# Kernel optimization log

Measured on AMD Instinct MI355X. Metric: run time of the kernel, lower is better.

The kernel has to match this reference:

```python
import jax, jax.numpy as jnp
import numpy as np

N_NODES = 10000
N_EDGES = 160000
N_FEAT = 512
HEADS = 8
HID = 128
OUT = 16


def setup_inputs() -> dict:
    key = jax.random.key(0)
    ks = jax.random.split(key, 16)
    inp = {
        'node_features': jax.random.normal(ks[0], (N_NODES, N_FEAT), jnp.float32),
        'edge_src': jax.random.randint(ks[1], (N_EDGES,), 0, N_NODES, jnp.int32),
        'edge_dst': jax.random.randint(ks[2], (N_EDGES,), 0, N_NODES, jnp.int32),
        # GAT layer params (scaled randn for numerical sanity)
        'W1': jax.random.normal(ks[3], (HEADS, HID, N_FEAT), jnp.float32) * 0.05,
        'a1': jax.random.normal(ks[4], (HEADS, 2 * HID), jnp.float32) * 0.05,
        'W2': jax.random.normal(ks[5], (HEADS, HID, HID), jnp.float32) * 0.05,
        'a2': jax.random.normal(ks[6], (HEADS, 2 * HID), jnp.float32) * 0.05,
        # MLP: LayerNorm(128) -> Linear(128,64) -> LeakyReLU -> Linear(64,16) -> LeakyReLU -> Linear(16,OUT) -> ReLU
        'ln_g': jnp.ones((HID,), jnp.float32),
        'ln_b': jnp.zeros((HID,), jnp.float32),
        'Wl1': jax.random.normal(ks[7], (64, HID), jnp.float32) * 0.05,
        'bl1': jnp.zeros((64,), jnp.float32),
        'Wl2': jax.random.normal(ks[8], (16, 64), jnp.float32) * 0.05,
        'bl2': jnp.zeros((16,), jnp.float32),
        'Wl3': jax.random.normal(ks[9], (OUT, 16), jnp.float32) * 0.05,
        'bl3': jnp.zeros((OUT,), jnp.float32),
    }
    return inp


def gat_layer(x, src, dst, W, a, n_nodes):
    # per-node, per-head projection: h[n,h,d]
    h = jnp.einsum('hdf,nf->nhd', W, x)
    # split attention vector: e_ij = a[:HID].h_i + a[HID:].h_j
    s_i = jnp.einsum('nhd,hd->nh', h, a[:, :HID])  # score contribution of target i
    s_j = jnp.einsum('nhd,hd->nh', h, a[:, HID:])  # score contribution of neighbor j
    e = jax.nn.leaky_relu(s_i[dst] + s_j[src])     # [E,H], negative_slope=0.01 (torch default)
    # segment softmax over edges grouped by dst
    m = jax.ops.segment_max(e, dst, num_segments=n_nodes)           # [N,H]
    m = jnp.where(jnp.isfinite(m), m, 0.0)
    ex = jnp.exp(e - m[dst])                                        # [E,H]
    denom = jax.ops.segment_sum(ex, dst, num_segments=n_nodes)      # [N,H]
    alpha = ex / jnp.where(denom > 0, denom, 1.0)[dst]              # [E,H]
    # scatter-accumulate weighted neighbor embeddings
    agg = jax.ops.segment_sum(alpha[:, :, None] * h[src], dst, num_segments=n_nodes)  # [N,H,HID]
    # average over heads, ELU (matches 1/attn_heads * attn_sum -> ELU)
    return jax.nn.elu(agg.mean(axis=1))  # [N,HID]


def reference(node_features, edge_src, edge_dst, W1, a1, W2, a2,
              ln_g, ln_b, Wl1, bl1, Wl2, bl2, Wl3, bl3):
    n = node_features.shape[0]
    emb1 = gat_layer(node_features, edge_src, edge_dst, W1, a1, n)
    emb2 = gat_layer(emb1, edge_src, edge_dst, W2, a2, n)
    g = emb2.mean(axis=0)  # [HID] graph embedding
    # MLP head (dropout = identity at inference)
    mu = g.mean()
    var = ((g - mu) ** 2).mean()
    gn = (g - mu) / jnp.sqrt(var + 1e-5) * ln_g + ln_b
    x = jax.nn.leaky_relu(Wl1 @ gn + bl1)
    x = jax.nn.leaky_relu(Wl2 @ x + bl2)
    return jax.nn.relu(Wl3 @ x + bl3)
```

## Files before the change

### kernel.cpp

```cpp
#include <hip/hip_runtime.h>
#include <math.h>

#define N_NODES 10000
#define N_EDGES 160000
#define N_FEAT  512
#define HEADS   8
#define HID     128

typedef __attribute__((ext_vector_type(8))) short bf16x8;
typedef __attribute__((ext_vector_type(4))) float f32x4;
typedef __attribute__((ext_vector_type(2))) float v2f;

__device__ inline unsigned short f2bf_rne(float f) {
  unsigned int u = __float_as_uint(f);
  unsigned int r = u + 0x7fffu + ((u >> 16) & 1u);
  return (unsigned short)(r >> 16);
}
__device__ inline float bf2f(unsigned int b) {
  return __uint_as_float(b << 16);
}

__device__ inline void split_body(const float* __restrict__ in,
                                  unsigned short* __restrict__ hi,
                                  int R, int K8, int idx) {
  int r = idx & 15;
  int t = idx >> 4;
  int kq = t % K8;
  int rb = t / K8;
  int row = rb * 16 + r;
  float v[8] = {0.f, 0.f, 0.f, 0.f, 0.f, 0.f, 0.f, 0.f};
  if (row < R) {
    const float* p = in + (size_t)row * (K8 * 8) + kq * 8;
    float4 a = *(const float4*)p;
    float4 b = *(const float4*)(p + 4);
    v[0] = a.x; v[1] = a.y; v[2] = a.z; v[3] = a.w;
    v[4] = b.x; v[5] = b.y; v[6] = b.z; v[7] = b.w;
  }
  union { unsigned short u[8]; int4 v4; } H;
  #pragma unroll
  for (int e = 0; e < 8; ++e) H.u[e] = f2bf_rne(v[e]);
  *(int4*)&hi[(size_t)idx * 8] = H.v4;
}

__global__ __launch_bounds__(256)
void split_frag2(const float* __restrict__ in1, unsigned short* __restrict__ hi1,
                 int R1, int K81, int total1, int nb1,
                 const float* __restrict__ in2, unsigned short* __restrict__ hi2,
                 int R2, int K82, int total2, int nb2,
                 const float* __restrict__ W2p, unsigned short* __restrict__ hi3,
                 int total3, int nb3,
                 const int* __restrict__ esrc, const int* __restrict__ edst,
                 int* __restrict__ deg, int* __restrict__ slots,
                 int2* __restrict__ ovf, int* __restrict__ cnt, int E,
                 const float* __restrict__ av1, const float* __restrict__ av2,
                 float* __restrict__ wt1, float* __restrict__ wt2) {
  int b = (int)blockIdx.x;
  int tid = threadIdx.x;
  if (b < nb1) {
    int idx = b * 256 + tid;
    if (idx < total1) split_body(in1, hi1, R1, K81, idx);
  } else if (b < nb1 + nb2) {
    int idx = (b - nb1) * 256 + tid;
    if (idx < total2) split_body(in2, hi2, R2, K82, idx);
  } else if (b < nb1 + nb2 + nb3) {
    int idx = (b - nb1 - nb2) * 256 + tid;
    if (idx < total3) split_body(W2p, hi3, HEADS * HID, 16, idx);
  } else {
    int nbE = (E + 255) / 256;
    int eb = b - nb1 - nb2 - nb3;
    if (eb < nbE) {
      int e = eb * 256 + tid;
      if (e < E) {
        int d = edst[e], s = esrc[e];
        int p = atomicAdd(&deg[d], 1);
        if (p < 32) {
          slots[d * 32 + p] = s;
        } else {
          int q = atomicAdd(&cnt[1], 1);
          if (q < E) ovf[q] = make_int2(d, s);
        }
      }
    } else {
      int wb = eb - nbE;
      if (wb < 32) {
        int o = wb * 256 + tid;
        int f = o & 511, ii = (o >> 9) & 1, h = o >> 10;
        const float* Wp = in2 + (size_t)h * HID * N_FEAT + f;
        const float* ap = av1 + h * 2 * HID + ii * HID;
        float c0 = 0.f, c1 = 0.f;
        for (int d = 0; d < HID; d += 2) {
          c0 = fmaf(Wp[(size_t)d * N_FEAT], ap[d], c0);
          c1 = fmaf(Wp[(size_t)(d + 1) * N_FEAT], ap[d + 1], c1);
        }
        wt1[o] = c0 + c1;
      } else {
        int o = (wb - 32) * 256 + tid;
        int f = o & 127, ii = (o >> 7) & 1, h = o >> 8;
        const float* Wp = W2p + (size_t)h * HID * HID + f;
        const float* ap = av2 + h * 2 * HID + ii * HID;
        float c0 = 0.f, c1 = 0.f;
        for (int d = 0; d < HID; d += 2) {
          c0 = fmaf(Wp[(size_t)d * HID], ap[d], c0);
          c1 = fmaf(Wp[(size_t)(d + 1) * HID], ap[d + 1], c1);
        }
        wt2[o] = c0 + c1;
      }
    }
  }
}

__global__ __launch_bounds__(256, 3)
void gemm_score(const unsigned short* __restrict__ Afh,
                const unsigned short* __restrict__ Bfh,
                unsigned short* __restrict__ hb,
                int M, int K, int nbGemm,
                const float* __restrict__ x, const float* __restrict__ wt1,
                float* __restrict__ si, float* __restrict__ sj, int N) {
  int tid = threadIdx.x;
  if ((int)blockIdx.x >= nbGemm) {
    __shared__ float wl[8192];
    #pragma unroll
    for (int k = 0; k < 32; ++k) wl[tid + k * 256] = wt1[tid + k * 256];
    __syncthreads();
    int wv = tid >> 6, lane = tid & 63;
    int rr = lane >> 4, sl = lane & 15;
    int n = ((int)blockIdx.x - nbGemm) * 16 + wv * 4 + rr;
    if (n >= N) return;
    const float* xp = x + (size_t)n * N_FEAT + sl * 4;
    float acc[16];
    #pragma unroll
    for (int t = 0; t < 16; ++t) acc[t] = 0.f;
    #pragma unroll
    for (int k = 0; k < 8; ++k) {
      float4 xv = *(const float4*)(xp + k * 64);
      #pragma unroll
      for (int t = 0; t < 16; ++t) {
        float4 w4 = *(const float4*)&wl[t * 512 + k * 64 + sl * 4];
        acc[t] = fmaf(xv.x, w4.x, fmaf(xv.y, w4.y, fmaf(xv.z, w4.z, fmaf(xv.w, w4.w, acc[t]))));
      }
    }
    #pragma unroll
    for (int o = 1; o <= 8; o <<= 1)
      #pragma unroll
      for (int t = 0; t < 16; ++t) acc[t] += __shfl_xor(acc[t], o);
    float outv = acc[0];
    #pragma unroll
    for (int t = 1; t < 16; ++t) outv = (sl == t) ? acc[t] : outv;
    int h = sl >> 1;
    if (sl & 1) sj[(size_t)h * N + n] = outv;
    else        si[(size_t)h * N + n] = outv;
    return;
  }

  int wave = tid >> 6, lane = tid & 63;
  int r = lane & 15, q = lane >> 4;
  int wr = wave >> 1, wc = wave & 1;

  int blk = blockIdx.x;
  int mtile = blk % 80;
  int head = blk / 80;
  int m0 = mtile * 128;
  int K8 = K >> 3;

  const bf16x8* pA = (const bf16x8*)Afh;
  const bf16x8* pB = (const bf16x8*)Bfh;
  size_t rstep = (size_t)K8 * 16;
  size_t aidx = (size_t)((m0 >> 4) + wr * 4) * rstep + (size_t)q * 16 + r;
  size_t bidx = (size_t)(head * 8 + wc * 4) * rstep + (size_t)q * 16 + r;

  f32x4 acc[4][4] = {};

  for (int k0 = 0; k0 < K; k0 += 64, aidx += 128, bidx += 128) {
    bf16x8 a[8], b[8];
    #pragma unroll
    for (int i = 0; i < 4; ++i) {
      a[i]     = pA[aidx + i * rstep];
      b[i]     = pB[bidx + i * rstep];
      a[i + 4] = pA[aidx + i * rstep + 64];
      b[i + 4] = pB[bidx + i * rstep + 64];
    }
    #pragma unroll
    for (int i = 0; i < 4; ++i)
      #pragma unroll
      for (int j = 0; j < 4; ++j)
        acc[i][j] = __builtin_amdgcn_mfma_f32_16x16x32_bf16(a[i], b[j], acc[i][j], 0, 0, 0);
    #pragma unroll
    for (int i = 0; i < 4; ++i)
      #pragma unroll
      for (int j = 0; j < 4; ++j)
        acc[i][j] = __builtin_amdgcn_mfma_f32_16x16x32_bf16(a[i + 4], b[j + 4], acc[i][j], 0, 0, 0);
  }

  #pragma unroll
  for (int i = 0; i < 4; ++i)
    #pragma unroll
    for (int reg = 0; reg < 4; ++reg) {
      int row = m0 + wr * 64 + i * 16 + q * 4 + reg;
      if (row < M) {
        #pragma unroll
        for (int j = 0; j < 4; ++j)
          hb[((size_t)head * M + row) * HID + wc * 64 + j * 16 + r] =
              f2bf_rne(acc[i][j][reg]);
      }
    }
}

__global__ __launch_bounds__(512)
void gat_aggregate9(const unsigned short* __restrict__ hb,
                    const float* __restrict__ si, const float* __restrict__ sj,
                    const int* __restrict__ deg, const int* __restrict__ slots,
                    const int2* __restrict__ ovf, const int* __restrict__ cnt,
                    unsigned short* __restrict__ aggb, int N) {
  __shared__ int2 prs[8][4][32];
  int head = blockIdx.x & 7;
  int wv = threadIdx.x >> 6;
  int lane = threadIdx.x & 63;
  int grp = lane >> 4;
  int sl = lane & 15;
  int n = (blockIdx.x >> 3) * 32 + wv * 4 + grp;
  const unsigned short* hbase = hb + (size_t)head * N * HID;
  const float* sjh = sj + (size_t)head * N;
  bool nv = n < N;
  int dg = 0;
  float s_i = 0.f;
  if (nv) {
    dg = deg[n];
    s_i = si[(size_t)head * N + n];
  }
  int sbase = n * 32;

  int src0 = 0, src1 = 0;
  float sc0 = -INFINITY, sc1 = -INFINITY;
  if (sl < dg) {
    src0 = slots[sbase + sl];
    float t = s_i + sjh[src0];
    sc0 = t > 0.f ? t : 0.01f * t;
  }
  if (16 + sl < dg) {
    src1 = slots[sbase + 16 + sl];
    float t = s_i + sjh[src1];
    sc1 = t > 0.f ? t : 0.01f * t;
  }
  float m = fmaxf(sc0, sc1);
  int oc = 0;
  if (dg > 32) {
    oc = cnt[1];
    if (oc > N_EDGES) oc = N_EDGES;
    for (int e2 = sl; e2 < oc; e2 += 16) {
      int2 pe = ovf[e2];
      if (pe.x == n) {
        float t = s_i + sjh[pe.y];
        t = t > 0.f ? t : 0.01f * t;
        m = fmaxf(m, t);
      }
    }
  }
  #pragma unroll
  for (int o = 1; o <= 8; o <<= 1) m = fmaxf(m, __shfl_xor(m, o));

  float w0 = (sl < dg) ? __expf(sc0 - m) : 0.f;
  float w1 = (16 + sl < dg) ? __expf(sc1 - m) : 0.f;
  float den = w0 + w1;
  if (dg > 32) {
    for (int e2 = sl; e2 < oc; e2 += 16) {
      int2 pe = ovf[e2];
      if (pe.x == n) {
        float t = s_i + sjh[pe.y];
        t = t > 0.f ? t : 0.01f * t;
        den += __expf(t - m);
      }
    }
  }
  #pragma unroll
  for (int o = 1; o <= 8; o <<= 1) den += __shfl_xor(den, o);

  prs[wv][grp][sl] = make_int2(src0, __float_as_int(w0));
  prs[wv][grp][16 + sl] = make_int2(src1, __float_as_int(w1));
  __asm__ volatile("s_waitcnt lgkmcnt(0)" ::: "memory");

  v2f a01 = {0.f, 0.f}, a23 = {0.f, 0.f}, a45 = {0.f, 0.f}, a67 = {0.f, 0.f};
  int dmin = dg < 32 ? dg : 32;
  for (int e0 = 0; e0 < dmin; e0 += 8) {
    int2 p[8];
    #pragma unroll
    for (int u = 0; u < 8; ++u) p[u] = prs[wv][grp][e0 + u];
    int4 pv[8];
    #pragma unroll
    for (int u = 0; u < 8; ++u)
      pv[u] = *(const int4*)&hbase[(size_t)p[u].x * HID + sl * 8];
    #pragma unroll
    for (int u = 0; u < 8; ++u) {
      float w = __int_as_float(p[u].y);
      v2f w2 = {w, w};
      int4 q = pv[u];
      v2f t0 = {bf2f((unsigned)q.x & 0xffffu), __uint_as_float((unsigned)q.x & 0xffff0000u)};
      v2f t1 = {bf2f((unsigned)q.y & 0xffffu), __uint_as_float((unsigned)q.y & 0xffff0000u)};
      v2f t2 = {bf2f((unsigned)q.z & 0xffffu), __uint_as_float((unsigned)q.z & 0xffff0000u)};
      v2f t3 = {bf2f((unsigned)q.w & 0xffffu), __uint_as_float((unsigned)q.w & 0xffff0000u)};
      a01 += w2 * t0;
      a23 += w2 * t1;
      a45 += w2 * t2;
      a67 += w2 * t3;
    }
  }
  if (dg > 32) {
    for (int e2 = 0; e2 < oc; ++e2) {
      int2 pe = ovf[e2];
      if (pe.x != n) continue;
      float t = s_i + sjh[pe.y];
      t = t > 0.f ? t : 0.01f * t;
      float w = __expf(t - m);
      v2f w2 = {w, w};
      int4 q = *(const int4*)&hbase[(size_t)pe.y * HID + sl * 8];
      v2f t0 = {bf2f((unsigned)q.x & 0xffffu), __uint_as_float((unsigned)q.x & 0xffff0000u)};
      v2f t1 = {bf2f((unsigned)q.y & 0xffffu), __uint_as_float((unsigned)q.y & 0xffff0000u)};
      v2f t2 = {bf2f((unsigned)q.z & 0xffffu), __uint_as_float((unsigned)q.z & 0xffff0000u)};
      v2f t3 = {bf2f((unsigned)q.w & 0xffffu), __uint_as_float((unsigned)q.w & 0xffff0000u)};
      a01 += w2 * t0; a23 += w2 * t1; a45 += w2 * t2; a67 += w2 * t3;
    }
  }

  if (nv) {
    float inv = den > 0.f ? 1.0f / den : 0.f;
    union { unsigned short u[8]; int4 v4; } P;
    P.u[0] = f2bf_rne(a01.x * inv); P.u[1] = f2bf_rne(a01.y * inv);
    P.u[2] = f2bf_rne(a23.x * inv); P.u[3] = f2bf_rne(a23.y * inv);
    P.u[4] = f2bf_rne(a45.x * inv); P.u[5] = f2bf_rne(a45.y * inv);
    P.u[6] = f2bf_rne(a67.x * inv); P.u[7] = f2bf_rne(a67.y * inv);
    *(int4*)&aggb[((size_t)head * N + n) * HID + sl * 8] = P.v4;
  }
}

__global__ __launch_bounds__(256)
void headmean_frag2(const unsigned short* __restrict__ aggb,
                    unsigned short* __restrict__ hiA, int N,
                    const float* __restrict__ wt2,
                    float* __restrict__ si, float* __restrict__ sj) {
  __shared__ float wl[2048];
  __shared__ float sred[16][16][17];
  int tid = threadIdx.x;
  #pragma unroll
  for (int k = 0; k < 8; ++k) wl[tid + k * 256] = wt2[tid + k * 256];
  __syncthreads();
  int idx = blockIdx.x * 256 + tid;
  int r = idx & 15;
  int kq = (idx >> 4) & 15;
  int rb = idx >> 8;
  int n = rb * 16 + r;
  float s[8] = {0.f, 0.f, 0.f, 0.f, 0.f, 0.f, 0.f, 0.f};
  if (n < N) {
    #pragma unroll
    for (int hh = 0; hh < HEADS; ++hh) {
      int4 pv = *(const int4*)&aggb[((size_t)hh * N + n) * HID + kq * 8];
      s[0] += bf2f((unsigned)pv.x & 0xffffu);
      s[1] += __uint_as_float((unsigned)pv.x & 0xffff0000u);
      s[2] += bf2f((unsigned)pv.y & 0xffffu);
      s[3] += __uint_as_float((unsigned)pv.y & 0xffff0000u);
      s[4] += bf2f((unsigned)pv.z & 0xffffu);
      s[5] += __uint_as_float((unsigned)pv.z & 0xffff0000u);
      s[6] += bf2f((unsigned)pv.w & 0xffffu);
      s[7] += __uint_as_float((unsigned)pv.w & 0xffff0000u);
    }
  }
  float p[16];
  #pragma unroll
  for (int t = 0; t < 16; ++t) p[t] = 0.f;
  union { unsigned short u[8]; int4 v4; } H;
  #pragma unroll
  for (int e = 0; e < 8; ++e) {
    float v = s[e] * (1.0f / HEADS);
    v = v > 0.f ? v : (__expf(v) - 1.0f);
    #pragma unroll
    for (int t = 0; t < 16; ++t) p[t] = fmaf(v, wl[t * 128 + kq * 8 + e], p[t]);
    H.u[e] = f2bf_rne(v);
  }
  *(int4*)&hiA[(size_t)idx * 8] = H.v4;
  #pragma unroll
  for (int t = 0; t < 16; ++t) sred[kq][r][t] = p[t];
  __syncthreads();
  {
    int rr = tid >> 4, t = tid & 15;
    float sum = 0.f;
    #pragma unroll
    for (int k = 0; k < 16; ++k) sum += sred[k][rr][t];
    int nn = rb * 16 + rr;
    if (nn < N) {
      int h = t >> 1;
      if (t & 1) sj[(size_t)h * N + nn] = sum;
      else       si[(size_t)h * N + nn] = sum;
    }
  }
}

__global__ __launch_bounds__(256)
void headmean_pool(const unsigned short* __restrict__ aggb, float* __restrict__ g,
                   int N) {
  __shared__ float sm[16][128];
  int t = threadIdx.x;
  int nl = t >> 4, dg = t & 15;
  int n = blockIdx.x * 16 + nl;
  float v[8] = {0.f, 0.f, 0.f, 0.f, 0.f, 0.f, 0.f, 0.f};
  if (n < N) {
    #pragma unroll
    for (int hh = 0; hh < HEADS; ++hh) {
      int4 pv = *(const int4*)&aggb[((size_t)hh * N + n) * HID + dg * 8];
      v[0] += bf2f((unsigned)pv.x & 0xffffu);
      v[1] += __uint_as_float((unsigned)pv.x & 0xffff0000u);
      v[2] += bf2f((unsigned)pv.y & 0xffffu);
      v[3] += __uint_as_float((unsigned)pv.y & 0xffff0000u);
      v[4] += bf2f((unsigned)pv.z & 0xffffu);
      v[5] += __uint_as_float((unsigned)pv.z & 0xffff0000u);
      v[6] += bf2f((unsigned)pv.w & 0xffffu);
      v[7] += __uint_as_float((unsigned)pv.w & 0xffff0000u);
    }
    #pragma unroll
    for (int e = 0; e < 8; ++e) {
      float x = v[e] * (1.0f / HEADS);
      v[e] = x > 0.f ? x : (__expf(x) - 1.0f);
    }
  }
  #pragma unroll
  for (int e = 0; e < 8; ++e) sm[nl][dg * 8 + e] = v[e];
  __syncthreads();
  if (t < 128) {
    float s = 0.f;
    #pragma unroll
    for (int nn = 0; nn < 16; ++nn) s += sm[nn][t];
    atomicAdd(&g[t], s);
  }
}

__global__ __launch_bounds__(128)
void mlp_kernel(const float* __restrict__ g, const float* __restrict__ ln_g,
                const float* __restrict__ ln_b, const float* __restrict__ Wl1,
                const float* __restrict__ bl1, const float* __restrict__ Wl2,
                const float* __restrict__ bl2, const float* __restrict__ Wl3,
                const float* __restrict__ bl3, float* __restrict__ out, float invN) {
  __shared__ float red[128];
  __shared__ float gn[128];
  __shared__ float x1[64];
  __shared__ float x2[16];
  int t = threadIdx.x;
  float gg = g[t] * invN;
  red[t] = gg;
  __syncthreads();
  for (int o = 64; o > 0; o >>= 1) {
    if (t < o) red[t] += red[t + o];
    __syncthreads();
  }
  float mu = red[0] * (1.0f / HID);
  __syncthreads();
  float dv = gg - mu;
  red[t] = dv * dv;
  __syncthreads();
  for (int o = 64; o > 0; o >>= 1) {
    if (t < o) red[t] += red[t + o];
    __syncthreads();
  }
  float var = red[0] * (1.0f / HID);
  gn[t] = dv / sqrtf(var + 1e-5f) * ln_g[t] + ln_b[t];
  __syncthreads();
  if (t < 64) {
    float s = bl1[t];
    for (int k = 0; k < 128; ++k) s += Wl1[t * 128 + k] * gn[k];
    x1[t] = s > 0.f ? s : 0.01f * s;
  }
  __syncthreads();
  if (t < 16) {
    float s = bl2[t];
    for (int k = 0; k < 64; ++k) s += Wl2[t * 64 + k] * x1[k];
    x2[t] = s > 0.f ? s : 0.01f * s;
  }
  __syncthreads();
  if (t < 16) {
    float s = bl3[t];
    for (int k = 0; k < 16; ++k) s += Wl3[t * 16 + k] * x2[k];
    out[t] = s > 0.f ? s : 0.f;
  }
}

extern "C" void kernel_launch(void* const* d_in, const int* in_sizes, int n_in,
                              void* d_out, int out_size, void* d_ws, size_t ws_size,
                              hipStream_t stream) {
  const float* x    = (const float*)d_in[0];
  const int*   esrc = (const int*)d_in[1];
  const int*   edst = (const int*)d_in[2];
  const float* W1   = (const float*)d_in[3];
  const float* a1   = (const float*)d_in[4];
  const float* W2   = (const float*)d_in[5];
  const float* a2   = (const float*)d_in[6];
  const float* ln_g = (const float*)d_in[7];
  const float* ln_b = (const float*)d_in[8];
  const float* Wl1  = (const float*)d_in[9];
  const float* bl1  = (const float*)d_in[10];
  const float* Wl2  = (const float*)d_in[11];
  const float* bl2  = (const float*)d_in[12];
  const float* Wl3  = (const float*)d_in[13];
  const float* bl3  = (const float*)d_in[14];
  float* out = (float*)d_out;

  const int RBPAD = 640;

  unsigned short* aggb = (unsigned short*)d_ws;
  float* si   = (float*)(aggb + (size_t)N_NODES * HEADS * HID);
  float* sj   = si + N_NODES * HEADS;
  float* g    = sj + N_NODES * HEADS;
  int*   deg  = (int*)(g + 128);
  int*   cnt  = deg + N_NODES;
  int*   slots= cnt + 4;
  int2*  ovf  = (int2*)(slots + (size_t)N_NODES * 32);
  float* wt1  = (float*)(ovf + N_EDGES);
  float* wt2  = wt1 + 8192;
  unsigned short* Afh  = (unsigned short*)(wt2 + 2048);
  unsigned short* Bfh  = Afh + (size_t)RBPAD * 64 * 128;
  unsigned short* Bfh2 = Bfh + (size_t)1024 * 512;
  unsigned short* hb   = Bfh2 + (size_t)1024 * 128;

  hipMemsetAsync(g, 0, 128 * sizeof(float) + (N_NODES + 4) * sizeof(int), stream);

  int gemmGrid = 80 * HEADS;
  int scoreGrid = (N_NODES + 15) / 16;
  int aggGrid = ((N_NODES + 31) / 32) * 8;

  {
    int totalA = RBPAD * 64 * 16;
    int nbA = (totalA + 255) / 256;
    int totalB = 64 * 64 * 16;
    int nbB = (totalB + 255) / 256;
    int totalB2 = 64 * 16 * 16;
    int nbB2 = (totalB2 + 255) / 256;
    int nbE = (N_EDGES + 255) / 256;
    int nbW = 40;
    split_frag2<<<nbA + nbB + nbB2 + nbE + nbW, 256, 0, stream>>>(
        x, Afh, N_NODES, 64, totalA, nbA,
        W1, Bfh, HEADS * HID, 64, totalB, nbB,
        W2, Bfh2, totalB2, nbB2,
        esrc, edst, deg, slots, ovf, cnt, N_EDGES,
        a1, a2, wt1, wt2);
  }

  gemm_score<<<gemmGrid + scoreGrid, 256, 0, stream>>>(
      Afh, Bfh, hb, N_NODES, N_FEAT, gemmGrid, x, wt1, si, sj, N_NODES);
  gat_aggregate9<<<aggGrid, 512, 0, stream>>>(hb, si, sj, deg, slots, ovf, cnt,
                                              aggb, N_NODES);
  headmean_frag2<<<(N_NODES + 15) / 16, 256, 0, stream>>>(aggb, Afh, N_NODES,
                                                          wt2, si, sj);

  gemm_score<<<gemmGrid, 256, 0, stream>>>(
      Afh, Bfh2, hb, N_NODES, HID, gemmGrid, nullptr, nullptr, nullptr, nullptr, 0);
  gat_aggregate9<<<aggGrid, 512, 0, stream>>>(hb, si, sj, deg, slots, ovf, cnt,
                                              aggb, N_NODES);

  headmean_pool<<<(N_NODES + 15) / 16, 256, 0, stream>>>(aggb, g, N_NODES);
  mlp_kernel<<<1, 128, 0, stream>>>(g, ln_g, ln_b, Wl1, bl1, Wl2, bl2, Wl3, bl3,
                                    out, 1.0f / N_NODES);
}
```

Baseline: 242.1 us.

## Fuse whole GAT pipeline into one persistent cooperative kernel with grid syncs

Replaces the seven separate kernel launches (prep/split, GEMM+score, aggregate, headmean, second GEMM, aggregate, pool, MLP) with a single cooperative persistent kernel of 256 or 512 blocks of 512 threads that loops over work items and separates phases with grid.sync(). The GEMM tile is reshaped for 8 waves per block (each wave now computes 32 rows instead of 64). The aim is to remove launch gaps and inter-kernel idle time. In exchange, the fixed grid may reduce parallelism in some phases, grid-wide barriers add cost, and the occupancy-dependent grid size carries risk.

```diff
diff --git a/kernel.cpp b/kernel.cpp
--- a/kernel.cpp
+++ b/kernel.cpp
@@ -1,5 +1,8 @@
 #include <hip/hip_runtime.h>
+#include <hip/hip_cooperative_groups.h>
 #include <math.h>
+
+namespace cg = cooperative_groups;
 
 #define N_NODES 10000
 #define N_EDGES 160000
@@ -42,160 +45,52 @@
   *(int4*)&hi[(size_t)idx * 8] = H.v4;
 }
 
-__global__ __launch_bounds__(256)
-void split_frag2(const float* __restrict__ in1, unsigned short* __restrict__ hi1,
-                 int R1, int K81, int total1, int nb1,
-                 const float* __restrict__ in2, unsigned short* __restrict__ hi2,
-                 int R2, int K82, int total2, int nb2,
-                 const float* __restrict__ W2p, unsigned short* __restrict__ hi3,
-                 int total3, int nb3,
-                 const int* __restrict__ esrc, const int* __restrict__ edst,
-                 int* __restrict__ deg, int* __restrict__ slots,
-                 int2* __restrict__ ovf, int* __restrict__ cnt, int E,
-                 const float* __restrict__ av1, const float* __restrict__ av2,
-                 float* __restrict__ wt1, float* __restrict__ wt2) {
-  int b = (int)blockIdx.x;
-  int tid = threadIdx.x;
-  if (b < nb1) {
-    int idx = b * 256 + tid;
-    if (idx < total1) split_body(in1, hi1, R1, K81, idx);
-  } else if (b < nb1 + nb2) {
-    int idx = (b - nb1) * 256 + tid;
-    if (idx < total2) split_body(in2, hi2, R2, K82, idx);
-  } else if (b < nb1 + nb2 + nb3) {
-    int idx = (b - nb1 - nb2) * 256 + tid;
-    if (idx < total3) split_body(W2p, hi3, HEADS * HID, 16, idx);
-  } else {
-    int nbE = (E + 255) / 256;
-    int eb = b - nb1 - nb2 - nb3;
-    if (eb < nbE) {
-      int e = eb * 256 + tid;
-      if (e < E) {
-        int d = edst[e], s = esrc[e];
-        int p = atomicAdd(&deg[d], 1);
-        if (p < 32) {
-          slots[d * 32 + p] = s;
-        } else {
-          int q = atomicAdd(&cnt[1], 1);
-          if (q < E) ovf[q] = make_int2(d, s);
-        }
-      }
-    } else {
-      int wb = eb - nbE;
-      if (wb < 32) {
-        int o = wb * 256 + tid;
-        int f = o & 511, ii = (o >> 9) & 1, h = o >> 10;
-        const float* Wp = in2 + (size_t)h * HID * N_FEAT + f;
-        const float* ap = av1 + h * 2 * HID + ii * HID;
-        float c0 = 0.f, c1 = 0.f;
-        for (int d = 0; d < HID; d += 2) {
-          c0 = fmaf(Wp[(size_t)d * N_FEAT], ap[d], c0);
-          c1 = fmaf(Wp[(size_t)(d + 1) * N_FEAT], ap[d + 1], c1);
-        }
-        wt1[o] = c0 + c1;
-      } else {
-        int o = (wb - 32) * 256 + tid;
-        int f = o & 127, ii = (o >> 7) & 1, h = o >> 8;
-        const float* Wp = W2p + (size_t)h * HID * HID + f;
-        const float* ap = av2 + h * 2 * HID + ii * HID;
-        float c0 = 0.f, c1 = 0.f;
-        for (int d = 0; d < HID; d += 2) {
-          c0 = fmaf(Wp[(size_t)d * HID], ap[d], c0);
-          c1 = fmaf(Wp[(size_t)(d + 1) * HID], ap[d + 1], c1);
-        }
-        wt2[o] = c0 + c1;
-      }
-    }
-  }
-}
-
-__global__ __launch_bounds__(256, 3)
-void gemm_score(const unsigned short* __restrict__ Afh,
-                const unsigned short* __restrict__ Bfh,
-                unsigned short* __restrict__ hb,
-                int M, int K, int nbGemm,
-                const float* __restrict__ x, const float* __restrict__ wt1,
-                float* __restrict__ si, float* __restrict__ sj, int N) {
-  int tid = threadIdx.x;
-  if ((int)blockIdx.x >= nbGemm) {
-    __shared__ float wl[8192];
-    #pragma unroll
-    for (int k = 0; k < 32; ++k) wl[tid + k * 256] = wt1[tid + k * 256];
-    __syncthreads();
-    int wv = tid >> 6, lane = tid & 63;
-    int rr = lane >> 4, sl = lane & 15;
-    int n = ((int)blockIdx.x - nbGemm) * 16 + wv * 4 + rr;
-    if (n >= N) return;
-    const float* xp = x + (size_t)n * N_FEAT + sl * 4;
-    float acc[16];
-    #pragma unroll
-    for (int t = 0; t < 16; ++t) acc[t] = 0.f;
-    #pragma unroll
-    for (int k = 0; k < 8; ++k) {
-      float4 xv = *(const float4*)(xp + k * 64);
-      #pragma unroll
-      for (int t = 0; t < 16; ++t) {
-        float4 w4 = *(const float4*)&wl[t * 512 + k * 64 + sl * 4];
-        acc[t] = fmaf(xv.x, w4.x, fmaf(xv.y, w4.y, fmaf(xv.z, w4.z, fmaf(xv.w, w4.w, acc[t]))));
-      }
-    }
-    #pragma unroll
-    for (int o = 1; o <= 8; o <<= 1)
-      #pragma unroll
-      for (int t = 0; t < 16; ++t) acc[t] += __shfl_xor(acc[t], o);
-    float outv = acc[0];
-    #pragma unroll
-    for (int t = 1; t < 16; ++t) outv = (sl == t) ? acc[t] : outv;
-    int h = sl >> 1;
-    if (sl & 1) sj[(size_t)h * N + n] = outv;
-    else        si[(size_t)h * N + n] = outv;
-    return;
-  }
-
+__device__ inline void gemm_tile_8w(const bf16x8* __restrict__ pA,
+                                    const bf16x8* __restrict__ pB,
+                                    unsigned short* __restrict__ hb,
+                                    int M, int K, int tile, int tid) {
   int wave = tid >> 6, lane = tid & 63;
   int r = lane & 15, q = lane >> 4;
   int wr = wave >> 1, wc = wave & 1;
-
-  int blk = blockIdx.x;
-  int mtile = blk % 80;
-  int head = blk / 80;
+  int mtile = tile % 80;
+  int head = tile / 80;
   int m0 = mtile * 128;
   int K8 = K >> 3;
-
-  const bf16x8* pA = (const bf16x8*)Afh;
-  const bf16x8* pB = (const bf16x8*)Bfh;
   size_t rstep = (size_t)K8 * 16;
-  size_t aidx = (size_t)((m0 >> 4) + wr * 4) * rstep + (size_t)q * 16 + r;
+  size_t aidx = (size_t)((m0 >> 4) + wr * 2) * rstep + (size_t)q * 16 + r;
   size_t bidx = (size_t)(head * 8 + wc * 4) * rstep + (size_t)q * 16 + r;
 
-  f32x4 acc[4][4] = {};
+  f32x4 acc[2][4] = {};
 
   for (int k0 = 0; k0 < K; k0 += 64, aidx += 128, bidx += 128) {
-    bf16x8 a[8], b[8];
-    #pragma unroll
-    for (int i = 0; i < 4; ++i) {
+    bf16x8 a[4], b[8];
+    #pragma unroll
+    for (int i = 0; i < 2; ++i) {
       a[i]     = pA[aidx + i * rstep];
-      b[i]     = pB[bidx + i * rstep];
-      a[i + 4] = pA[aidx + i * rstep + 64];
-      b[i + 4] = pB[bidx + i * rstep + 64];
-    }
-    #pragma unroll
-    for (int i = 0; i < 4; ++i)
+      a[i + 2] = pA[aidx + i * rstep + 64];
+    }
+    #pragma unroll
+    for (int j = 0; j < 4; ++j) {
+      b[j]     = pB[bidx + j * rstep];
+      b[j + 4] = pB[bidx + j * rstep + 64];
+    }
+    #pragma unroll
+    for (int i = 0; i < 2; ++i)
       #pragma unroll
       for (int j = 0; j < 4; ++j)
         acc[i][j] = __builtin_amdgcn_mfma_f32_16x16x32_bf16(a[i], b[j], acc[i][j], 0, 0, 0);
     #pragma unroll
-    for (int i = 0; i < 4; ++i)
+    for (int i = 0; i < 2; ++i)
       #pragma unroll
       for (int j = 0; j < 4; ++j)
-        acc[i][j] = __builtin_amdgcn_mfma_f32_16x16x32_bf16(a[i + 4], b[j + 4], acc[i][j], 0, 0, 0);
+        acc[i][j] = __builtin_amdgcn_mfma_f32_16x16x32_bf16(a[i + 2], b[j + 4], acc[i][j], 0, 0, 0);
   }
 
   #pragma unroll
-  for (int i = 0; i < 4; ++i)
+  for (int i = 0; i < 2; ++i)
     #pragma unroll
     for (int reg = 0; reg < 4; ++reg) {
-      int row = m0 + wr * 64 + i * 16 + q * 4 + reg;
+      int row = m0 + wr * 32 + i * 16 + q * 4 + reg;
       if (row < M) {
         #pragma unroll
         for (int j = 0; j < 4; ++j)
@@ -205,277 +100,396 @@
     }
 }
 
-__global__ __launch_bounds__(512)
-void gat_aggregate9(const unsigned short* __restrict__ hb,
-                    const float* __restrict__ si, const float* __restrict__ sj,
-                    const int* __restrict__ deg, const int* __restrict__ slots,
-                    const int2* __restrict__ ovf, const int* __restrict__ cnt,
-                    unsigned short* __restrict__ aggb, int N) {
-  __shared__ int2 prs[8][4][32];
-  int head = blockIdx.x & 7;
-  int wv = threadIdx.x >> 6;
-  int lane = threadIdx.x & 63;
+__device__ inline void agg_phase(const unsigned short* __restrict__ hb,
+                                 const float* __restrict__ si,
+                                 const float* __restrict__ sj,
+                                 const int* __restrict__ deg,
+                                 const int* __restrict__ slots,
+                                 const int2* __restrict__ ovf,
+                                 const int* __restrict__ cnt,
+                                 unsigned short* __restrict__ aggb,
+                                 char* smem, int tid, int bid, int nblk) {
+  int2 (*prs)[4][32] = (int2 (*)[4][32])smem;
+  int wv = tid >> 6;
+  int lane = tid & 63;
   int grp = lane >> 4;
   int sl = lane & 15;
-  int n = (blockIdx.x >> 3) * 32 + wv * 4 + grp;
-  const unsigned short* hbase = hb + (size_t)head * N * HID;
-  const float* sjh = sj + (size_t)head * N;
-  bool nv = n < N;
-  int dg = 0;
-  float s_i = 0.f;
-  if (nv) {
-    dg = deg[n];
-    s_i = si[(size_t)head * N + n];
-  }
-  int sbase = n * 32;
-
-  int src0 = 0, src1 = 0;
-  float sc0 = -INFINITY, sc1 = -INFINITY;
-  if (sl < dg) {
-    src0 = slots[sbase + sl];
-    float t = s_i + sjh[src0];
-    sc0 = t > 0.f ? t : 0.01f * t;
-  }
-  if (16 + sl < dg) {
-    src1 = slots[sbase + 16 + sl];
-    float t = s_i + sjh[src1];
-    sc1 = t > 0.f ? t : 0.01f * t;
-  }
-  float m = fmaxf(sc0, sc1);
-  int oc = 0;
-  if (dg > 32) {
-    oc = cnt[1];
-    if (oc > N_EDGES) oc = N_EDGES;
-    for (int e2 = sl; e2 < oc; e2 += 16) {
-      int2 pe = ovf[e2];
-      if (pe.x == n) {
+  for (int vb = bid; vb < 313 * 8; vb += nblk) {
+    int head = vb & 7;
+    int n = (vb >> 3) * 32 + wv * 4 + grp;
+    const unsigned short* hbase = hb + (size_t)head * N_NODES * HID;
+    const float* sjh = sj + (size_t)head * N_NODES;
+    bool nv = n < N_NODES;
+    int dg = 0;
+    float s_i = 0.f;
+    if (nv) {
+      dg = deg[n];
+      s_i = si[(size_t)head * N_NODES + n];
+    }
+    int sbase = n * 32;
+
+    int src0 = 0, src1 = 0;
+    float sc0 = -INFINITY, sc1 = -INFINITY;
+    if (sl < dg) {
+      src0 = slots[sbase + sl];
+      float t = s_i + sjh[src0];
+      sc0 = t > 0.f ? t : 0.01f * t;
+    }
+    if (16 + sl < dg) {
+      src1 = slots[sbase + 16 + sl];
+      float t = s_i + sjh[src1];
+      sc1 = t > 0.f ? t : 0.01f * t;
+    }
+    float m = fmaxf(sc0, sc1);
+    int oc = 0;
+    if (dg > 32) {
+      oc = cnt[1];
+      if (oc > N_EDGES) oc = N_EDGES;
+      for (int e2 = sl; e2 < oc; e2 += 16) {
+        int2 pe = ovf[e2];
+        if (pe.x == n) {
+          float t = s_i + sjh[pe.y];
+          t = t > 0.f ? t : 0.01f * t;
+          m = fmaxf(m, t);
+        }
+      }
+    }
+    #pragma unroll
+    for (int o = 1; o <= 8; o <<= 1) m = fmaxf(m, __shfl_xor(m, o));
+
+    float w0 = (sl < dg) ? __expf(sc0 - m) : 0.f;
+    float w1 = (16 + sl < dg) ? __expf(sc1 - m) : 0.f;
+    float den = w0 + w1;
+    if (dg > 32) {
+      for (int e2 = sl; e2 < oc; e2 += 16) {
+        int2 pe = ovf[e2];
+        if (pe.x == n) {
+          float t = s_i + sjh[pe.y];
+          t = t > 0.f ? t : 0.01f * t;
+          den += __expf(t - m);
+        }
+      }
+    }
+    #pragma unroll
+    for (int o = 1; o <= 8; o <<= 1) den += __shfl_xor(den, o);
+
+    prs[wv][grp][sl] = make_int2(src0, __float_as_int(w0));
+    prs[wv][grp][16 + sl] = make_int2(src1, __float_as_int(w1));
+    __asm__ volatile("s_waitcnt lgkmcnt(0)" ::: "memory");
+
+    v2f a01 = {0.f, 0.f}, a23 = {0.f, 0.f}, a45 = {0.f, 0.f}, a67 = {0.f, 0.f};
+    int dmin = dg < 32 ? dg : 32;
+    for (int e0 = 0; e0 < dmin; e0 += 8) {
+      int2 p[8];
+      #pragma unroll
+      for (int u = 0; u < 8; ++u) p[u] = prs[wv][grp][e0 + u];
+      int4 pv[8];
+      #pragma unroll
+      for (int u = 0; u < 8; ++u)
+        pv[u] = *(const int4*)&hbase[(size_t)p[u].x * HID + sl * 8];
+      #pragma unroll
+      for (int u = 0; u < 8; ++u) {
+        float w = __int_as_float(p[u].y);
+        v2f w2 = {w, w};
+        int4 q = pv[u];
+        v2f t0 = {bf2f((unsigned)q.x & 0xffffu), __uint_as_float((unsigned)q.x & 0xffff0000u)};
+        v2f t1 = {bf2f((unsigned)q.y & 0xffffu), __uint_as_float((unsigned)q.y & 0xffff0000u)};
+        v2f t2 = {bf2f((unsigned)q.z & 0xffffu), __uint_as_float((unsigned)q.z & 0xffff0000u)};
+        v2f t3 = {bf2f((unsigned)q.w & 0xffffu), __uint_as_float((unsigned)q.w & 0xffff0000u)};
+        a01 += w2 * t0;
+        a23 += w2 * t1;
+        a45 += w2 * t2;
+        a67 += w2 * t3;
+      }
+    }
+    if (dg > 32) {
+      for (int e2 = 0; e2 < oc; ++e2) {
+        int2 pe = ovf[e2];
+        if (pe.x != n) continue;
         float t = s_i + sjh[pe.y];
         t = t > 0.f ? t : 0.01f * t;
-        m = fmaxf(m, t);
-      }
-    }
-  }
-  #pragma unroll
-  for (int o = 1; o <= 8; o <<= 1) m = fmaxf(m, __shfl_xor(m, o));
-
-  float w0 = (sl < dg) ? __expf(sc0 - m) : 0.f;
-  float w1 = (16 + sl < dg) ? __expf(sc1 - m) : 0.f;
-  float den = w0 + w1;
-  if (dg > 32) {
-    for (int e2 = sl; e2 < oc; e2 += 16) {
-      int2 pe = ovf[e2];
-      if (pe.x == n) {
-        float t = s_i + sjh[pe.y];
-        t = t > 0.f ? t : 0.01f * t;
-        den += __expf(t - m);
-      }
-    }
-  }
-  #pragma unroll
-  for (int o = 1; o <= 8; o <<= 1) den += __shfl_xor(den, o);
-
-  prs[wv][grp][sl] = make_int2(src0, __float_as_int(w0));
-  prs[wv][grp][16 + sl] = make_int2(src1, __float_as_int(w1));
-  __asm__ volatile("s_waitcnt lgkmcnt(0)" ::: "memory");
-
-  v2f a01 = {0.f, 0.f}, a23 = {0.f, 0.f}, a45 = {0.f, 0.f}, a67 = {0.f, 0.f};
-  int dmin = dg < 32 ? dg : 32;
-  for (int e0 = 0; e0 < dmin; e0 += 8) {
-    int2 p[8];
-    #pragma unroll
-    for (int u = 0; u < 8; ++u) p[u] = prs[wv][grp][e0 + u];
-    int4 pv[8];
-    #pragma unroll
-    for (int u = 0; u < 8; ++u)
-      pv[u] = *(const int4*)&hbase[(size_t)p[u].x * HID + sl * 8];
-    #pragma unroll
-    for (int u = 0; u < 8; ++u) {
-      float w = __int_as_float(p[u].y);
-      v2f w2 = {w, w};
-      int4 q = pv[u];
-      v2f t0 = {bf2f((unsigned)q.x & 0xffffu), __uint_as_float((unsigned)q.x & 0xffff0000u)};
-      v2f t1 = {bf2f((unsigned)q.y & 0xffffu), __uint_as_float((unsigned)q.y & 0xffff0000u)};
-      v2f t2 = {bf2f((unsigned)q.z & 0xffffu), __uint_as_float((unsigned)q.z & 0xffff0000u)};
-      v2f t3 = {bf2f((unsigned)q.w & 0xffffu), __uint_as_float((unsigned)q.w & 0xffff0000u)};
-      a01 += w2 * t0;
-      a23 += w2 * t1;
-      a45 += w2 * t2;
-      a67 += w2 * t3;
-    }
-  }
-  if (dg > 32) {
-    for (int e2 = 0; e2 < oc; ++e2) {
-      int2 pe = ovf[e2];
-      if (pe.x != n) continue;
-      float t = s_i + sjh[pe.y];
-      t = t > 0.f ? t : 0.01f * t;
-      float w = __expf(t - m);
-      v2f w2 = {w, w};
-      int4 q = *(const int4*)&hbase[(size_t)pe.y * HID + sl * 8];
-      v2f t0 = {bf2f((unsigned)q.x & 0xffffu), __uint_as_float((unsigned)q.x & 0xffff0000u)};
-      v2f t1 = {bf2f((unsigned)q.y & 0xffffu), __uint_as_float((unsigned)q.y & 0xffff0000u)};
-      v2f t2 = {bf2f((unsigned)q.z & 0xffffu), __uint_as_float((unsigned)q.z & 0xffff0000u)};
-      v2f t3 = {bf2f((unsigned)q.w & 0xffffu), __uint_as_float((unsigned)q.w & 0xffff0000u)};
-      a01 += w2 * t0; a23 += w2 * t1; a45 += w2 * t2; a67 += w2 * t3;
-    }
-  }
-
-  if (nv) {
-    float inv = den > 0.f ? 1.0f / den : 0.f;
-    union { unsigned short u[8]; int4 v4; } P;
-    P.u[0] = f2bf_rne(a01.x * inv); P.u[1] = f2bf_rne(a01.y * inv);
-    P.u[2] = f2bf_rne(a23.x * inv); P.u[3] = f2bf_rne(a23.y * inv);
-    P.u[4] = f2bf_rne(a45.x * inv); P.u[5] = f2bf_rne(a45.y * inv);
-    P.u[6] = f2bf_rne(a67.x * inv); P.u[7] = f2bf_rne(a67.y * inv);
-    *(int4*)&aggb[((size_t)head * N + n) * HID + sl * 8] = P.v4;
-  }
-}
-
-__global__ __launch_bounds__(256)
-void headmean_frag2(const unsigned short* __restrict__ aggb,
-                    unsigned short* __restrict__ hiA, int N,
-                    const float* __restrict__ wt2,
-                    float* __restrict__ si, float* __restrict__ sj) {
-  __shared__ float wl[2048];
-  __shared__ float sred[16][16][17];
-  int tid = threadIdx.x;
-  #pragma unroll
-  for (int k = 0; k < 8; ++k) wl[tid + k * 256] = wt2[tid + k * 256];
-  __syncthreads();
-  int idx = blockIdx.x * 256 + tid;
-  int r = idx & 15;
-  int kq = (idx >> 4) & 15;
-  int rb = idx >> 8;
-  int n = rb * 16 + r;
-  float s[8] = {0.f, 0.f, 0.f, 0.f, 0.f, 0.f, 0.f, 0.f};
-  if (n < N) {
-    #pragma unroll
-    for (int hh = 0; hh < HEADS; ++hh) {
-      int4 pv = *(const int4*)&aggb[((size_t)hh * N + n) * HID + kq * 8];
-      s[0] += bf2f((unsigned)pv.x & 0xffffu);
-      s[1] += __uint_as_float((unsigned)pv.x & 0xffff0000u);
-      s[2] += bf2f((unsigned)pv.y & 0xffffu);
-      s[3] += __uint_as_float((unsigned)pv.y & 0xffff0000u);
-      s[4] += bf2f((unsigned)pv.z & 0xffffu);
-      s[5] += __uint_as_float((unsigned)pv.z & 0xffff0000u);
-      s[6] += bf2f((unsigned)pv.w & 0xffffu);
-      s[7] += __uint_as_float((unsigned)pv.w & 0xffff0000u);
-    }
-  }
-  float p[16];
-  #pragma unroll
-  for (int t = 0; t < 16; ++t) p[t] = 0.f;
-  union { unsigned short u[8]; int4 v4; } H;
-  #pragma unroll
-  for (int e = 0; e < 8; ++e) {
-    float v = s[e] * (1.0f / HEADS);
-    v = v > 0.f ? v : (__expf(v) - 1.0f);
-    #pragma unroll
-    for (int t = 0; t < 16; ++t) p[t] = fmaf(v, wl[t * 128 + kq * 8 + e], p[t]);
-    H.u[e] = f2bf_rne(v);
-  }
-  *(int4*)&hiA[(size_t)idx * 8] = H.v4;
-  #pragma unroll
-  for (int t = 0; t < 16; ++t) sred[kq][r][t] = p[t];
-  __syncthreads();
+        float w = __expf(t - m);
+        v2f w2 = {w, w};
+        int4 q = *(const int4*)&hbase[(size_t)pe.y * HID + sl * 8];
+        v2f t0 = {bf2f((unsigned)q.x & 0xffffu), __uint_as_float((unsigned)q.x & 0xffff0000u)};
+        v2f t1 = {bf2f((unsigned)q.y & 0xffffu), __uint_as_float((unsigned)q.y & 0xffff0000u)};
+        v2f t2 = {bf2f((unsigned)q.z & 0xffffu), __uint_as_float((unsigned)q.z & 0xffff0000u)};
+        v2f t3 = {bf2f((unsigned)q.w & 0xffffu), __uint_as_float((unsigned)q.w & 0xffff0000u)};
+        a01 += w2 * t0; a23 += w2 * t1; a45 += w2 * t2; a67 += w2 * t3;
+      }
+    }
+
+    if (nv) {
+      float inv = den > 0.f ? 1.0f / den : 0.f;
+      union { unsigned short u[8]; int4 v4; } P;
+      P.u[0] = f2bf_rne(a01.x * inv); P.u[1] = f2bf_rne(a01.y * inv);
+      P.u[2] = f2bf_rne(a23.x * inv); P.u[3] = f2bf_rne(a23.y * inv);
+      P.u[4] = f2bf_rne(a45.x * inv); P.u[5] = f2bf_rne(a45.y * inv);
+      P.u[6] = f2bf_rne(a67.x * inv); P.u[7] = f2bf_rne(a67.y * inv);
+      *(int4*)&aggb[((size_t)head * N_NODES + n) * HID + sl * 8] = P.v4;
+    }
+  }
+}
+
+__global__ __launch_bounds__(512, 4)
+void fused_gat(const float* __restrict__ x, const int* __restrict__ esrc,
+               const int* __restrict__ edst,
+               const float* __restrict__ W1, const float* __restrict__ a1,
+               const float* __restrict__ W2, const float* __restrict__ a2,
+               const float* __restrict__ ln_g, const float* __restrict__ ln_b,
+               const float* __restrict__ Wl1, const float* __restrict__ bl1,
+               const float* __restrict__ Wl2, const float* __restrict__ bl2,
+               const float* __restrict__ Wl3, const float* __restrict__ bl3,
+               float* __restrict__ out,
+               unsigned short* __restrict__ aggb, float* __restrict__ si,
+               float* __restrict__ sj, float* __restrict__ g,
+               int* __restrict__ deg, int* __restrict__ cnt,
+               int* __restrict__ slots, int2* __restrict__ ovf,
+               float* __restrict__ wt1, float* __restrict__ wt2,
+               unsigned short* __restrict__ Afh, unsigned short* __restrict__ Bfh,
+               unsigned short* __restrict__ Bfh2, unsigned short* __restrict__ hb) {
+  __shared__ __align__(16) char smem[43264];
+  cg::grid_group grid = cg::this_grid();
+  const int tid = threadIdx.x;
+  const int bid = blockIdx.x;
+  const int nblk = gridDim.x;
+  const int gtid = bid * 512 + tid;
+  const int gstride = nblk * 512;
+
+  for (int idx = gtid; idx < 640 * 64 * 16; idx += gstride)
+    split_body(x, Afh, N_NODES, 64, idx);
+  for (int idx = gtid; idx < 64 * 64 * 16; idx += gstride)
+    split_body(W1, Bfh, HEADS * HID, 64, idx);
+  for (int idx = gtid; idx < 64 * 16 * 16; idx += gstride)
+    split_body(W2, Bfh2, HEADS * HID, 16, idx);
+  for (int e = gtid; e < N_EDGES; e += gstride) {
+    int d = edst[e], s = esrc[e];
+    int p = atomicAdd(&deg[d], 1);
+    if (p < 32) {
+      slots[d * 32 + p] = s;
+    } else {
+      int q = atomicAdd(&cnt[1], 1);
+      if (q < N_EDGES) ovf[q] = make_int2(d, s);
+    }
+  }
+  for (int o = gtid; o < 8192; o += gstride) {
+    int f = o & 511, ii = (o >> 9) & 1, h = o >> 10;
+    const float* Wp = W1 + (size_t)h * HID * N_FEAT + f;
+    const float* ap = a1 + h * 2 * HID + ii * HID;
+    float c0 = 0.f, c1 = 0.f;
+    for (int d = 0; d < HID; d += 2) {
+      c0 = fmaf(Wp[(size_t)d * N_FEAT], ap[d], c0);
+      c1 = fmaf(Wp[(size_t)(d + 1) * N_FEAT], ap[d + 1], c1);
+    }
+    wt1[o] = c0 + c1;
+  }
+  for (int o = gtid; o < 2048; o += gstride) {
+    int f = o & 127, ii = (o >> 7) & 1, h = o >> 8;
+    const float* Wp = W2 + (size_t)h * HID * HID + f;
+    const float* ap = a2 + h * 2 * HID + ii * HID;
+    float c0 = 0.f, c1 = 0.f;
+    for (int d = 0; d < HID; d += 2) {
+      c0 = fmaf(Wp[(size_t)d * HID], ap[d], c0);
+      c1 = fmaf(Wp[(size_t)(d + 1) * HID], ap[d + 1], c1);
+    }
+    wt2[o] = c0 + c1;
+  }
+  grid.sync();
+
+  for (int t = bid; t < 640; t += nblk)
+    gemm_tile_8w((const bf16x8*)Afh, (const bf16x8*)Bfh, hb, N_NODES, N_FEAT, t, tid);
   {
-    int rr = tid >> 4, t = tid & 15;
-    float sum = 0.f;
-    #pragma unroll
-    for (int k = 0; k < 16; ++k) sum += sred[k][rr][t];
-    int nn = rb * 16 + rr;
-    if (nn < N) {
-      int h = t >> 1;
-      if (t & 1) sj[(size_t)h * N + nn] = sum;
-      else       si[(size_t)h * N + nn] = sum;
-    }
-  }
-}
-
-__global__ __launch_bounds__(256)
-void headmean_pool(const unsigned short* __restrict__ aggb, float* __restrict__ g,
-                   int N) {
-  __shared__ float sm[16][128];
-  int t = threadIdx.x;
-  int nl = t >> 4, dg = t & 15;
-  int n = blockIdx.x * 16 + nl;
-  float v[8] = {0.f, 0.f, 0.f, 0.f, 0.f, 0.f, 0.f, 0.f};
-  if (n < N) {
-    #pragma unroll
-    for (int hh = 0; hh < HEADS; ++hh) {
-      int4 pv = *(const int4*)&aggb[((size_t)hh * N + n) * HID + dg * 8];
-      v[0] += bf2f((unsigned)pv.x & 0xffffu);
-      v[1] += __uint_as_float((unsigned)pv.x & 0xffff0000u);
-      v[2] += bf2f((unsigned)pv.y & 0xffffu);
-      v[3] += __uint_as_float((unsigned)pv.y & 0xffff0000u);
-      v[4] += bf2f((unsigned)pv.z & 0xffffu);
-      v[5] += __uint_as_float((unsigned)pv.z & 0xffff0000u);
-      v[6] += bf2f((unsigned)pv.w & 0xffffu);
-      v[7] += __uint_as_float((unsigned)pv.w & 0xffff0000u);
-    }
-    #pragma unroll
-    for (int e = 0; e < 8; ++e) {
-      float x = v[e] * (1.0f / HEADS);
-      v[e] = x > 0.f ? x : (__expf(x) - 1.0f);
-    }
-  }
-  #pragma unroll
-  for (int e = 0; e < 8; ++e) sm[nl][dg * 8 + e] = v[e];
-  __syncthreads();
-  if (t < 128) {
-    float s = 0.f;
-    #pragma unroll
-    for (int nn = 0; nn < 16; ++nn) s += sm[nn][t];
-    atomicAdd(&g[t], s);
-  }
-}
-
-__global__ __launch_bounds__(128)
-void mlp_kernel(const float* __restrict__ g, const float* __restrict__ ln_g,
-                const float* __restrict__ ln_b, const float* __restrict__ Wl1,
-                const float* __restrict__ bl1, const float* __restrict__ Wl2,
-                const float* __restrict__ bl2, const float* __restrict__ Wl3,
-                const float* __restrict__ bl3, float* __restrict__ out, float invN) {
-  __shared__ float red[128];
-  __shared__ float gn[128];
-  __shared__ float x1[64];
-  __shared__ float x2[16];
-  int t = threadIdx.x;
-  float gg = g[t] * invN;
-  red[t] = gg;
-  __syncthreads();
-  for (int o = 64; o > 0; o >>= 1) {
-    if (t < o) red[t] += red[t + o];
-    __syncthreads();
-  }
-  float mu = red[0] * (1.0f / HID);
-  __syncthreads();
-  float dv = gg - mu;
-  red[t] = dv * dv;
-  __syncthreads();
-  for (int o = 64; o > 0; o >>= 1) {
-    if (t < o) red[t] += red[t + o];
-    __syncthreads();
-  }
-  float var = red[0] * (1.0f / HID);
-  gn[t] = dv / sqrtf(var + 1e-5f) * ln_g[t] + ln_b[t];
-  __syncthreads();
-  if (t < 64) {
-    float s = bl1[t];
-    for (int k = 0; k < 128; ++k) s += Wl1[t * 128 + k] * gn[k];
-    x1[t] = s > 0.f ? s : 0.01f * s;
-  }
-  __syncthreads();
-  if (t < 16) {
-    float s = bl2[t];
-    for (int k = 0; k < 64; ++k) s += Wl2[t * 64 + k] * x1[k];
-    x2[t] = s > 0.f ? s : 0.01f * s;
-  }
-  __syncthreads();
-  if (t < 16) {
-    float s = bl3[t];
-    for (int k = 0; k < 16; ++k) s += Wl3[t * 16 + k] * x2[k];
-    out[t] = s > 0.f ? s : 0.f;
+    float* wl = (float*)smem;
+    for (int k = tid; k < 8192; k += 512) wl[k] = wt1[k];
+    __syncthreads();
+    int wv = tid >> 6, lane = tid & 63;
+    int rr = lane >> 4, sl = lane & 15;
+    for (int vb = bid; vb < 313; vb += nblk) {
+      int n = vb * 32 + wv * 4 + rr;
+      float acc[16];
+      #pragma unroll
+      for (int t = 0; t < 16; ++t) acc[t] = 0.f;
+      if (n < N_NODES) {
+        const float* xp = x + (size_t)n * N_FEAT + sl * 4;
+        #pragma unroll
+        for (int k = 0; k < 8; ++k) {
+          float4 xv = *(const float4*)(xp + k * 64);
+          #pragma unroll
+          for (int t = 0; t < 16; ++t) {
+            float4 w4 = *(const float4*)&wl[t * 512 + k * 64 + sl * 4];
+            acc[t] = fmaf(xv.x, w4.x, fmaf(xv.y, w4.y, fmaf(xv.z, w4.z, fmaf(xv.w, w4.w, acc[t]))));
+          }
+        }
+      }
+      #pragma unroll
+      for (int o = 1; o <= 8; o <<= 1)
+        #pragma unroll
+        for (int t = 0; t < 16; ++t) acc[t] += __shfl_xor(acc[t], o);
+      if (n < N_NODES) {
+        float outv = acc[0];
+        #pragma unroll
+        for (int t = 1; t < 16; ++t) outv = (sl == t) ? acc[t] : outv;
+        int h = sl >> 1;
+        if (sl & 1) sj[(size_t)h * N_NODES + n] = outv;
+        else        si[(size_t)h * N_NODES + n] = outv;
+      }
+    }
+  }
+  grid.sync();
+
+  agg_phase(hb, si, sj, deg, slots, ovf, cnt, aggb, smem, tid, bid, nblk);
+  grid.sync();
+
+  {
+    float* wl2 = (float*)smem;
+    float (*sred)[32][17] = (float (*)[32][17])(smem + 8192);
+    for (int k = tid; k < 2048; k += 512) wl2[k] = wt2[k];
+    __syncthreads();
+    int kq = tid >> 5, r32 = tid & 31;
+    for (int vb = bid; vb < 313; vb += nblk) {
+      int n = vb * 32 + r32;
+      float s[8] = {0.f, 0.f, 0.f, 0.f, 0.f, 0.f, 0.f, 0.f};
+      if (n < N_NODES) {
+        #pragma unroll
+        for (int hh = 0; hh < HEADS; ++hh) {
+          int4 pv = *(const int4*)&aggb[((size_t)hh * N_NODES + n) * HID + kq * 8];
+          s[0] += bf2f((unsigned)pv.x & 0xffffu);
+          s[1] += __uint_as_float((unsigned)pv.x & 0xffff0000u);
+          s[2] += bf2f((unsigned)pv.y & 0xffffu);
+          s[3] += __uint_as_float((unsigned)pv.y & 0xffff0000u);
+          s[4] += bf2f((unsigned)pv.z & 0xffffu);
+          s[5] += __uint_as_float((unsigned)pv.z & 0xffff0000u);
+          s[6] += bf2f((unsigned)pv.w & 0xffffu);
+          s[7] += __uint_as_float((unsigned)pv.w & 0xffff0000u);
+        }
+      }
+      float p[16];
+      #pragma unroll
+      for (int t = 0; t < 16; ++t) p[t] = 0.f;
+      union { unsigned short u[8]; int4 v4; } H;
+      #pragma unroll
+      for (int e = 0; e < 8; ++e) {
+        float v = s[e] * (1.0f / HEADS);
+        v = v > 0.f ? v : (__expf(v) - 1.0f);
+        #pragma unroll
+        for (int t = 0; t < 16; ++t) p[t] = fmaf(v, wl2[t * 128 + kq * 8 + e], p[t]);
+        H.u[e] = f2bf_rne(v);
+      }
+      if (n < N_NODES) {
+        size_t idx = ((size_t)(n >> 4) * 16 + kq) * 16 + (n & 15);
+        *(int4*)&Afh[idx * 8] = H.v4;
+      }
+      #pragma unroll
+      for (int t = 0; t < 16; ++t) sred[kq][r32][t] = p[t];
+      __syncthreads();
+      {
+        int rr = tid >> 4, t = tid & 15;
+        float sum = 0.f;
+        #pragma unroll
+        for (int k = 0; k < 16; ++k) sum += sred[k][rr][t];
+        int nn = vb * 32 + rr;
+        if (nn < N_NODES) {
+          int h = t >> 1;
+          if (t & 1) sj[(size_t)h * N_NODES + nn] = sum;
+          else       si[(size_t)h * N_NODES + nn] = sum;
+        }
+      }
+      __syncthreads();
+    }
+  }
+  grid.sync();
+
+  for (int t = bid; t < 640; t += nblk)
+    gemm_tile_8w((const bf16x8*)Afh, (const bf16x8*)Bfh2, hb, N_NODES, HID, t, tid);
+  grid.sync();
+
+  agg_phase(hb, si, sj, deg, slots, ovf, cnt, aggb, smem, tid, bid, nblk);
+  grid.sync();
+
+  {
+    float (*sm)[128] = (float (*)[128])smem;
+    int nl = tid >> 4, dgx = tid & 15;
+    for (int vb = bid; vb < 313; vb += nblk) {
+      int n = vb * 32 + nl;
+      float v[8] = {0.f, 0.f, 0.f, 0.f, 0.f, 0.f, 0.f, 0.f};
+      if (n < N_NODES) {
+        #pragma unroll
+        for (int hh = 0; hh < HEADS; ++hh) {
+          int4 pv = *(const int4*)&aggb[((size_t)hh * N_NODES + n) * HID + dgx * 8];
+          v[0] += bf2f((unsigned)pv.x & 0xffffu);
+          v[1] += __uint_as_float((unsigned)pv.x & 0xffff0000u);
+          v[2] += bf2f((unsigned)pv.y & 0xffffu);
+          v[3] += __uint_as_float((unsigned)pv.y & 0xffff0000u);
+          v[4] += bf2f((unsigned)pv.z & 0xffffu);
+          v[5] += __uint_as_float((unsigned)pv.z & 0xffff0000u);
+          v[6] += bf2f((unsigned)pv.w & 0xffffu);
+          v[7] += __uint_as_float((unsigned)pv.w & 0xffff0000u);
+        }
+        #pragma unroll
+        for (int e = 0; e < 8; ++e) {
+          float xv = v[e] * (1.0f / HEADS);
+          v[e] = xv > 0.f ? xv : (__expf(xv) - 1.0f);
+        }
+      }
+      #pragma unroll
+      for (int e = 0; e < 8; ++e) sm[nl][dgx * 8 + e] = v[e];
+      __syncthreads();
+      if (tid < 128) {
+        float s = 0.f;
+        #pragma unroll
+        for (int nn = 0; nn < 32; ++nn) s += sm[nn][tid];
+        atomicAdd(&g[tid], s);
+      }
+      __syncthreads();
+    }
+  }
+  grid.sync();
+
+  if (bid == 0) {
+    float* red = (float*)smem;
+    float* gnb = red + 128;
+    float* x1 = gnb + 128;
+    float* x2 = x1 + 64;
+    int t = tid;
+    float gg = 0.f;
+    if (t < 128) {
+      gg = g[t] * (1.0f / N_NODES);
+      red[t] = gg;
+    }
+    __syncthreads();
+    for (int o = 64; o > 0; o >>= 1) {
+      if (t < o) red[t] += red[t + o];
+      __syncthreads();
+    }
+    float mu = red[0] * (1.0f / HID);
+    __syncthreads();
+    if (t < 128) red[t] = (gg - mu) * (gg - mu);
+    __syncthreads();
+    for (int o = 64; o > 0; o >>= 1) {
+      if (t < o) red[t] += red[t + o];
+      __syncthreads();
+    }
+    float var = red[0] * (1.0f / HID);
+    __syncthreads();
+    if (t < 128) gnb[t] = (gg - mu) / sqrtf(var + 1e-5f) * ln_g[t] + ln_b[t];
+    __syncthreads();
+    if (t < 64) {
+      float s = bl1[t];
+      for (int k = 0; k < 128; ++k) s += Wl1[t * 128 + k] * gnb[k];
+      x1[t] = s > 0.f ? s : 0.01f * s;
+    }
+    __syncthreads();
+    if (t < 16) {
+      float s = bl2[t];
+      for (int k = 0; k < 64; ++k) s += Wl2[t * 64 + k] * x1[k];
+      x2[t] = s > 0.f ? s : 0.01f * s;
+    }
+    __syncthreads();
+    if (t < 16) {
+      float s = bl3[t];
+      for (int k = 0; k < 16; ++k) s += Wl3[t * 16 + k] * x2[k];
+      out[t] = s > 0.f ? s : 0.f;
+    }
   }
 }
 
@@ -518,40 +532,22 @@
 
   hipMemsetAsync(g, 0, 128 * sizeof(float) + (N_NODES + 4) * sizeof(int), stream);
 
-  int gemmGrid = 80 * HEADS;
-  int scoreGrid = (N_NODES + 15) / 16;
-  int aggGrid = ((N_NODES + 31) / 32) * 8;
-
-  {
-    int totalA = RBPAD * 64 * 16;
-    int nbA = (totalA + 255) / 256;
-    int totalB = 64 * 64 * 16;
-    int nbB = (totalB + 255) / 256;
-    int totalB2 = 64 * 16 * 16;
-    int nbB2 = (totalB2 + 255) / 256;
-    int nbE = (N_EDGES + 255) / 256;
-    int nbW = 40;
-    split_frag2<<<nbA + nbB + nbB2 + nbE + nbW, 256, 0, stream>>>(
-        x, Afh, N_NODES, 64, totalA, nbA,
-        W1, Bfh, HEADS * HID, 64, totalB, nbB,
-        W2, Bfh2, totalB2, nbB2,
-        esrc, edst, deg, slots, ovf, cnt, N_EDGES,
-        a1, a2, wt1, wt2);
-  }
-
-  gemm_score<<<gemmGrid + scoreGrid, 256, 0, stream>>>(
-      Afh, Bfh, hb, N_NODES, N_FEAT, gemmGrid, x, wt1, si, sj, N_NODES);
-  gat_aggregate9<<<aggGrid, 512, 0, stream>>>(hb, si, sj, deg, slots, ovf, cnt,
-                                              aggb, N_NODES);
-  headmean_frag2<<<(N_NODES + 15) / 16, 256, 0, stream>>>(aggb, Afh, N_NODES,
-                                                          wt2, si, sj);
-
-  gemm_score<<<gemmGrid, 256, 0, stream>>>(
-      Afh, Bfh2, hb, N_NODES, HID, gemmGrid, nullptr, nullptr, nullptr, nullptr, 0);
-  gat_aggregate9<<<aggGrid, 512, 0, stream>>>(hb, si, sj, deg, slots, ovf, cnt,
-                                              aggb, N_NODES);
-
-  headmean_pool<<<(N_NODES + 15) / 16, 256, 0, stream>>>(aggb, g, N_NODES);
-  mlp_kernel<<<1, 128, 0, stream>>>(g, ln_g, ln_b, Wl1, bl1, Wl2, bl2, Wl3, bl3,
-                                    out, 1.0f / N_NODES);
-}
+  int maxB = 0;
+  if (hipOccupancyMaxActiveBlocksPerMultiprocessor(&maxB, fused_gat, 512, 0)
+          != hipSuccess || maxB < 1)
+    maxB = 1;
+  int gridSz = (maxB >= 2) ? 512 : 256;
+
+  void* args[] = {
+    (void*)&x, (void*)&esrc, (void*)&edst, (void*)&W1, (void*)&a1,
+    (void*)&W2, (void*)&a2, (void*)&ln_g, (void*)&ln_b,
+    (void*)&Wl1, (void*)&bl1, (void*)&Wl2, (void*)&bl2,
+    (void*)&Wl3, (void*)&bl3, (void*)&out,
+    (void*)&aggb, (void*)&si, (void*)&sj, (void*)&g,
+    (void*)&deg, (void*)&cnt, (void*)&slots, (void*)&ovf,
+    (void*)&wt1, (void*)&wt2, (void*)&Afh, (void*)&Bfh,
+    (void*)&Bfh2, (void*)&hb
+  };
+  hipLaunchCooperativeKernel((const void*)fused_gat, dim3(gridSz), dim3(512),
+                             args, 0, stream);
+}
```

Result: slower. 539.4 us (+122.9%).
